# Kernel tuning notes

Measured on AMD Instinct MI355X. Metric: run time of the kernel, lower is better.

## Reference

```python
import jax, jax.numpy as jnp
import numpy as np

N_NODES = 16384
N_EDGES = 262144
D = 300
N_GRAPHS = 64


def setup_inputs() -> dict:
    key = jax.random.key(0)
    ks = jax.random.split(key, 16)
    s = 0.05  # small init scale for numerical stability
    inp = {
        "node_feats": jax.random.normal(ks[0], (N_NODES, D), jnp.float32),
        "W_lift": jax.random.normal(ks[1], (D, D), jnp.float32) * s,
        "b_lift": jnp.zeros((D,), jnp.float32),
        "Wf1": jax.random.normal(ks[2], (D, D), jnp.float32) * s,
        "bf1": jnp.zeros((D,), jnp.float32),
        "Wo1": jax.random.normal(ks[3], (D, D), jnp.float32) * s,
        "bo1": jnp.zeros((D,), jnp.float32),
        "Wf2": jax.random.normal(ks[4], (D, D), jnp.float32) * s,
        "bf2": jnp.zeros((D,), jnp.float32),
        "Wo2": jax.random.normal(ks[5], (D, D), jnp.float32) * s,
        "bo2": jnp.zeros((D,), jnp.float32),
        "Wf3": jax.random.normal(ks[6], (D, D), jnp.float32) * s,
        "bf3": jnp.zeros((D,), jnp.float32),
        "Wo3": jax.random.normal(ks[7], (D, D), jnp.float32) * s,
        "bo3": jnp.zeros((D,), jnp.float32),
        "W_ro": jax.random.normal(ks[8], (D, 2), jnp.float32) * s,
        "b_ro": jnp.zeros((2,), jnp.float32),
        "src": jax.random.randint(ks[9], (N_EDGES,), 0, N_NODES, jnp.int32),
        "dst": jax.random.randint(ks[10], (N_EDGES,), 0, N_NODES, jnp.int32),
        "graph_ids": jnp.sort(jax.random.randint(ks[11], (N_NODES,), 0, N_GRAPHS, jnp.int32)),
    }
    return inp


def _mp_layer(h, Wf, bf, Wo, bo, src, dst):
    # message: relu Dense on gathered src feats; reduce: segment-sum into dst nodes
    msg = jax.nn.relu(h[src] @ Wf + bf)                      # [E, D]
    agg = jax.ops.segment_sum(msg, dst, num_segments=N_NODES)  # [N, D]
    return jax.nn.relu(agg @ Wo + bo)                        # output Dense+ReLU


def reference(node_feats, W_lift, b_lift, Wf1, bf1, Wo1, bo1, Wf2, bf2, Wo2, bo2,
              Wf3, bf3, Wo3, bo3, W_ro, b_ro, src, dst, graph_ids):
    h = node_feats @ W_lift + b_lift  # lift, no activation
    h = _mp_layer(h, Wf1, bf1, Wo1, bo1, src, dst)
    h = _mp_layer(h, Wf2, bf2, Wo2, bo2, src, dst)
    h = _mp_layer(h, Wf3, bf3, Wo3, bo3, src, dst)
    probs = jax.nn.softmax(h @ W_ro + b_ro, axis=-1)         # readout Dense(softmax)
    logits = jax.ops.segment_sum(probs, graph_ids, num_segments=N_GRAPHS)  # dgl.sum_nodes
    return logits
```

## Files before the change

### kernel.cpp

```cpp
#include <hip/hip_runtime.h>
#include <hip/hip_bf16.h>

#define N_NODES 16384
#define N_EDGES 262144
#define GD 300
#define DP 320
#define N_GRAPHS 64
#define NTILE 5

typedef short bf16x8 __attribute__((ext_vector_type(8)));
typedef float f32x4 __attribute__((ext_vector_type(4)));

__device__ static inline unsigned short f2bf(float v) {
  __hip_bfloat16 b = __float2bfloat16(v);
  return __builtin_bit_cast(unsigned short, b);
}
__device__ static inline float bf2f(unsigned short u) {
  return __bfloat162float(__builtin_bit_cast(__hip_bfloat16, u));
}

#define GLOAD_LDS16(g, l)                                                    \
  __builtin_amdgcn_global_load_lds(                                          \
      (const __attribute__((address_space(1))) void*)(g),                    \
      (__attribute__((address_space(3))) void*)(l), 16, 0, 0)

constexpr int ATILE = 8192;
constexpr int AFULL = 5 * ATILE;
constexpr int BBUF = 40960;
constexpr int EPITCH = 328;
constexpr size_t WSZ = (size_t)DP * DP;
static_assert(64 * EPITCH * 2 <= AFULL + 2 * BBUF, "epilogue bounce fits");

template <bool RELU1, bool TILED, bool FUSE2, bool RO, bool CONVF>
__global__ __launch_bounds__(512, 2) void gemm_f(
    const unsigned short* __restrict__ A, const float* __restrict__ nf,
    const unsigned short* __restrict__ Wt1,
    const float* __restrict__ bias1, const unsigned short* __restrict__ Wt2,
    const float* __restrict__ bias2, unsigned short* __restrict__ C,
    const float* __restrict__ Wro, const float* __restrict__ bro,
    const int* __restrict__ gid, float* __restrict__ out) {
  __shared__ __align__(16) char smem[AFULL + 2 * BBUF];
  __shared__ float wroL[2 * DP];
  __shared__ float rowacc[2 * 64];
  __shared__ float binsL[2 * N_GRAPHS];

  const int bm = blockIdx.x * 64;
  const int t = threadIdx.x;
  const int w = t >> 6, l = t & 63;
  const int wr = w & 1;
  const int wc = w >> 1;
  const int cl = l & 15, q = l >> 4;
  const int lr = l >> 3;
  const int sg = (l & 7) ^ lr;

  if (RO) {
    for (int i = t; i < DP; i += 512) {
      wroL[2 * i] = (i < GD) ? Wro[2 * i] : 0.f;
      wroL[2 * i + 1] = (i < GD) ? Wro[2 * i + 1] : 0.f;
    }
    if (t < 128) rowacc[t] = 0.f;
    if (t < 2 * N_GRAPHS) binsL[t] = 0.f;
  }

  auto stageB = [&](const unsigned short* W, int tk, int buf) {
    char* lb = smem + AFULL + buf * BBUF;
#pragma unroll
    for (int i = 0; i < 5; ++i) {
      int c = w + 8 * i;
      GLOAD_LDS16(W + (size_t)(c * 8 + lr) * DP + tk * 64 + 8 * sg,
                  lb + c * 1024);
    }
  };

  f32x4 acc[2][5] = {};

  auto compute = [&](const char* lA, const char* lB) {
#pragma unroll
    for (int ks = 0; ks < 2; ++ks) {
      bf16x8 a[2], b[5];
#pragma unroll
      for (int m = 0; m < 2; ++m) {
        int r = wr * 32 + m * 16 + cl;
        int slot = (ks * 4 + q) ^ (r & 7);
        a[m] = *(const bf16x8*)(lA + r * 128 + slot * 16);
      }
#pragma unroll
      for (int n = 0; n < 5; ++n) {
        int r = wc * 80 + n * 16 + cl;
        int slot = (ks * 4 + q) ^ (r & 7);
        b[n] = *(const bf16x8*)(lB + r * 128 + slot * 16);
      }
#pragma unroll
      for (int m = 0; m < 2; ++m)
#pragma unroll
        for (int n = 0; n < 5; ++n)
          acc[m][n] = __builtin_amdgcn_mfma_f32_16x16x32_bf16(a[m], b[n],
                                                              acc[m][n], 0, 0, 0);
    }
  };

  stageB(Wt1, 0, 0);
  if (CONVF) {
    const int r = t >> 3;
    const int ls = t & 7;
    const float* rp = nf + (size_t)(bm + r) * GD;
#pragma unroll
    for (int p = 0; p < 5; ++p) {
      int c0 = p * 64 + ls * 8;
      bf16x8 o;
      if (c0 + 8 <= GD) {
        float4 a = *(const float4*)(rp + c0);
        float4 b = *(const float4*)(rp + c0 + 4);
        o[0] = f2bf(a.x); o[1] = f2bf(a.y); o[2] = f2bf(a.z); o[3] = f2bf(a.w);
        o[4] = f2bf(b.x); o[5] = f2bf(b.y); o[6] = f2bf(b.z); o[7] = f2bf(b.w);
      } else {
#pragma unroll
        for (int i = 0; i < 8; ++i) {
          int c = c0 + i;
          o[i] = f2bf(c < GD ? rp[c] : 0.f);
        }
      }
      *(bf16x8*)(smem + p * ATILE + r * 128 + ((ls ^ (r & 7)) << 4)) = o;
    }
    asm volatile("s_waitcnt lgkmcnt(0)" ::: "memory");
  } else {
#pragma unroll
    for (int p = 0; p < 5; ++p)
      GLOAD_LDS16(A + (size_t)(bm + w * 8 + lr) * DP + p * 64 + 8 * sg,
                  smem + p * ATILE + w * 1024);
  }

  for (int tk = 0; tk < 5; ++tk) {
    __builtin_amdgcn_s_barrier();
    if (tk + 1 < 5) {
      stageB(Wt1, tk + 1, (tk + 1) & 1);
      asm volatile("s_waitcnt vmcnt(5)" ::: "memory");
    } else {
      asm volatile("s_waitcnt vmcnt(0)" ::: "memory");
    }
    __builtin_amdgcn_s_barrier();
    compute(smem + tk * ATILE, smem + AFULL + (tk & 1) * BBUF);
  }

  if (FUSE2) {
    __syncthreads();
    stageB(Wt2, 0, 0);
#pragma unroll
    for (int n = 0; n < 5; ++n) {
      int col = wc * 80 + n * 16 + cl;
      float bv = bias1[col];
      int kt = col >> 6, kin = col & 63;
#pragma unroll
      for (int m = 0; m < 2; ++m) {
#pragma unroll
        for (int r = 0; r < 4; ++r) {
          int row = wr * 32 + m * 16 + q * 4 + r;
          float v = fmaxf(acc[m][n][r] + bv, 0.f);
          int byte = kt * ATILE + row * 128 + (((kin >> 3) ^ (row & 7)) << 4) +
                     ((kin & 7) << 1);
          *(unsigned short*)(smem + byte) = f2bf(v);
        }
      }
    }
    asm volatile("s_waitcnt lgkmcnt(0)" ::: "memory");
#pragma unroll
    for (int m = 0; m < 2; ++m)
#pragma unroll
      for (int n = 0; n < 5; ++n) acc[m][n] = f32x4{0.f, 0.f, 0.f, 0.f};

    for (int tk = 0; tk < 5; ++tk) {
      __builtin_amdgcn_s_barrier();
      if (tk + 1 < 5) {
        stageB(Wt2, tk + 1, (tk + 1) & 1);
        asm volatile("s_waitcnt vmcnt(5)" ::: "memory");
      } else {
        asm volatile("s_waitcnt vmcnt(0)" ::: "memory");
      }
      __builtin_amdgcn_s_barrier();
      compute(smem + tk * ATILE, smem + AFULL + (tk & 1) * BBUF);
    }
  }

  if (!RO) {
    const float* bp = FUSE2 ? bias2 : bias1;
    const bool relu = FUSE2 ? true : RELU1;
    __syncthreads();
    unsigned short* ep = (unsigned short*)smem;
#pragma unroll
    for (int n = 0; n < 5; ++n) {
      int col = wc * 80 + n * 16 + cl;
      float bv = bp[col];
#pragma unroll
      for (int m = 0; m < 2; ++m) {
#pragma unroll
        for (int r = 0; r < 4; ++r) {
          int row = wr * 32 + m * 16 + q * 4 + r;
          float v = acc[m][n][r] + bv;
          if (relu) v = fmaxf(v, 0.f);
          ep[row * EPITCH + col] = f2bf(v);
        }
      }
    }
    __syncthreads();
    {
      const int row = t >> 3, c0 = (t & 7) * 40;
#pragma unroll
      for (int gch = 0; gch < 5; ++gch) {
        int col = c0 + gch * 8;
        bf16x8 v = *(const bf16x8*)(ep + row * EPITCH + col);
        size_t idx;
        if (TILED)
          idx = ((size_t)(col >> 6) * N_NODES + (bm + row)) * 64 + (col & 63);
        else
          idx = (size_t)(bm + row) * DP + col;
        *(bf16x8*)(C + idx) = v;
      }
    }
  } else {
    float bv[5];
#pragma unroll
    for (int n = 0; n < 5; ++n) bv[n] = bias1[wc * 80 + n * 16 + cl];
#pragma unroll
    for (int m = 0; m < 2; ++m) {
#pragma unroll
      for (int r = 0; r < 4; ++r) {
        float s0 = 0.f, s1 = 0.f;
#pragma unroll
        for (int n = 0; n < 5; ++n) {
          int col = wc * 80 + n * 16 + cl;
          float v = fmaxf(acc[m][n][r] + bv[n], 0.f);
          s0 += v * wroL[2 * col];
          s1 += v * wroL[2 * col + 1];
        }
#pragma unroll
        for (int off = 1; off < 16; off <<= 1) {
          s0 += __shfl_xor(s0, off);
          s1 += __shfl_xor(s1, off);
        }
        if (cl == 0) {
          int row = wr * 32 + m * 16 + q * 4 + r;
          atomicAdd(&rowacc[2 * row], s0);
          atomicAdd(&rowacc[2 * row + 1], s1);
        }
      }
    }
    __syncthreads();
    if (t < 64) {
      float d0 = rowacc[2 * t] + bro[0];
      float d1 = rowacc[2 * t + 1] + bro[1];
      float mx = fmaxf(d0, d1);
      float e0 = expf(d0 - mx), e1 = expf(d1 - mx);
      float inv = 1.f / (e0 + e1);
      int g = gid[bm + t];
      atomicAdd(&binsL[2 * g], e0 * inv);
      atomicAdd(&binsL[2 * g + 1], e1 * inv);
    }
    __syncthreads();
    if (t < 2 * N_GRAPHS) {
      float v = binsL[t];
      if (v != 0.f) atomicAdd(&out[t], v);
    }
  }
}

__global__ void hist_kernel(const int* __restrict__ dst, int* __restrict__ cnt) {
  int e = blockIdx.x * blockDim.x + threadIdx.x;
  if (e < N_EDGES) atomicAdd(&cnt[dst[e]], 1);
}

__global__ __launch_bounds__(256) void scan_kernel(
    const int* __restrict__ cnt, int* __restrict__ row_ptr, int* __restrict__ row_fill,
    float* __restrict__ out, int out_n) {
  if (threadIdx.x < out_n) out[threadIdx.x] = 0.f;
  __shared__ int sums[256];
  const int t = threadIdx.x;
  const int base = t * 64;
  int loc[64];
#pragma unroll
  for (int i = 0; i < 16; ++i)
    *(int4*)&loc[i * 4] = *(const int4*)&cnt[base + i * 4];
  int s = 0;
#pragma unroll
  for (int i = 0; i < 64; ++i) s += loc[i];
  sums[t] = s;
  __syncthreads();
  for (int off = 1; off < 256; off <<= 1) {
    int x = (t >= off) ? sums[t - off] : 0;
    __syncthreads();
    sums[t] += x;
    __syncthreads();
  }
  int run = sums[t] - s;
  int rp[64];
#pragma unroll
  for (int i = 0; i < 64; ++i) {
    rp[i] = run;
    run += loc[i];
  }
#pragma unroll
  for (int i = 0; i < 16; ++i) {
    *(int4*)&row_ptr[base + i * 4] = *(const int4*)&rp[i * 4];
    *(int4*)&row_fill[base + i * 4] = *(const int4*)&rp[i * 4];
  }
  if (t == 255) row_ptr[N_NODES] = run;
}

__global__ void scatter_kernel(const int* __restrict__ src, const int* __restrict__ dst,
                               int* __restrict__ row_fill, int* __restrict__ csr_src) {
  int e = blockIdx.x * blockDim.x + threadIdx.x;
  if (e >= N_EDGES) return;
  int pos = atomicAdd(&row_fill[dst[e]], 1);
  csr_src[pos] = src[e];
}

__global__ __launch_bounds__(256) void spmm_tiled(
    const unsigned short* __restrict__ Mt, const int* __restrict__ row_ptr,
    const int* __restrict__ csr_src, unsigned short* __restrict__ agg) {
  const int tile = blockIdx.y;
  const int wv = threadIdx.x >> 6;
  const int l = threadIdx.x & 63;
  const int g = l >> 3;
  const int cs = l & 7;
  const int node = blockIdx.x * 32 + wv * 8 + g;
  const unsigned short* base = Mt + (size_t)tile * N_NODES * 64 + cs * 8;

  int j = row_ptr[node];
  const int j1 = row_ptr[node + 1];
  float acc[8] = {};
  for (; j + 8 <= j1; j += 8) {
    bf16x8 v[8];
#pragma unroll
    for (int u = 0; u < 8; ++u)
      v[u] = *(const bf16x8*)(base + (size_t)csr_src[j + u] * 64);
#pragma unroll
    for (int u = 0; u < 8; ++u)
#pragma unroll
      for (int i = 0; i < 8; ++i) acc[i] += bf2f(v[u][i]);
  }
  if (j + 4 <= j1) {
    bf16x8 v[4];
#pragma unroll
    for (int u = 0; u < 4; ++u)
      v[u] = *(const bf16x8*)(base + (size_t)csr_src[j + u] * 64);
#pragma unroll
    for (int u = 0; u < 4; ++u)
#pragma unroll
      for (int i = 0; i < 8; ++i) acc[i] += bf2f(v[u][i]);
    j += 4;
  }
  for (; j < j1; ++j) {
    bf16x8 v = *(const bf16x8*)(base + (size_t)csr_src[j] * 64);
#pragma unroll
    for (int i = 0; i < 8; ++i) acc[i] += bf2f(v[i]);
  }
  bf16x8 o;
#pragma unroll
  for (int i = 0; i < 8; ++i) o[i] = f2bf(acc[i]);
  *(bf16x8*)(agg + (size_t)node * DP + tile * 64 + cs * 8) = o;
}

struct WPtrs {
  const float* W[7];
  const float* b[5];
};

__global__ __launch_bounds__(256) void prep_kernel(
    WPtrs p, const float* __restrict__ bl, const float* __restrict__ bf1,
    unsigned short* __restrict__ Wt, float* __restrict__ biasP,
    int* __restrict__ cnt) {
  __shared__ unsigned short ld[64][33];
  const int t = threadIdx.x;
  const int wb = blockIdx.x;

  if (wb < 64) cnt[wb * 256 + t] = 0;

  if (wb >= 350) {
    __shared__ float red[4][64];
    const int b = wb - 350;
    const int nn = t & 63, jg = t >> 6;
    const int n = b * 64 + nn;
    const float* Wf1 = p.W[0];
    float s = 0.f;
    if (n < GD) {
      for (int j = jg; j < GD; j += 4) s += bl[j] * Wf1[(size_t)j * GD + n];
    }
    red[jg][nn] = s;
    __syncthreads();
    if (t < 64) {
      int nn2 = b * 64 + t;
      float v = red[0][t] + red[1][t] + red[2][t] + red[3][t];
      biasP[nn2] = (nn2 < GD) ? v + bf1[nn2] : 0.f;
      biasP[DP + nn2] = 0.f;
    }
    return;
  }

  const int wi = wb / 50;
  const int blk = wb - wi * 50;
  const int kt = blk / 5;
  const int nt = blk - kt * 5;
  const int k0 = kt * 32, n0 = nt * 64;
  const float* W = p.W[wi];

  if (wi == 6) {
#pragma unroll
    for (int ps = 0; ps < 8; ++ps) {
      int idx = t + 256 * ps;
      int rr = idx >> 6, cc = idx & 63;
      float v = (k0 + rr < GD && n0 + cc < GD) ? W[(size_t)(k0 + rr) * GD + n0 + cc] : 0.f;
      Wt[2 * WSZ + (size_t)(k0 + rr) * DP + n0 + cc] = f2bf(v);
    }
    return;
  }
  const int slot = (wi == 0) ? 1 : wi + 2;
#pragma unroll
  for (int ps = 0; ps < 8; ++ps) {
    int idx = t + 256 * ps;
    int rr = idx >> 6, cc = idx & 63;
    float v = (k0 + rr < GD && n0 + cc < GD) ? W[(size_t)(k0 + rr) * GD + n0 + cc] : 0.f;
    ld[cc][rr] = f2bf(v);
  }
  __syncthreads();
#pragma unroll
  for (int ps = 0; ps < 8; ++ps) {
    int idx = t + 256 * ps;
    int nn = idx >> 5, kk = idx & 31;
    Wt[(size_t)slot * WSZ + (size_t)(n0 + nn) * DP + k0 + kk] = ld[nn][kk];
  }
  if (blk == 0 && wi >= 1) {
    for (int i = t; i < DP; i += 256)
      biasP[(size_t)(wi + 2) * DP + i] = (i < GD) ? p.b[wi - 1][i] : 0.f;
  }
}

extern "C" void kernel_launch(void* const* d_in, const int* in_sizes, int n_in,
                              void* d_out, int out_size, void* d_ws, size_t ws_size,
                              hipStream_t stream) {
  const float* node_feats = (const float*)d_in[0];
  const float* W_lift = (const float*)d_in[1];
  const float* b_lift = (const float*)d_in[2];
  const float* Wf1 = (const float*)d_in[3];
  const float* bf1 = (const float*)d_in[4];
  const float* W_ro = (const float*)d_in[15];
  const float* b_ro = (const float*)d_in[16];
  const int* src = (const int*)d_in[17];
  const int* dst = (const int*)d_in[18];
  const int* gid = (const int*)d_in[19];
  float* out = (float*)d_out;

  WPtrs wp;
  wp.W[0] = Wf1;
  wp.W[1] = (const float*)d_in[5];   wp.b[0] = (const float*)d_in[6];
  wp.W[2] = (const float*)d_in[7];   wp.b[1] = (const float*)d_in[8];
  wp.W[3] = (const float*)d_in[9];   wp.b[2] = (const float*)d_in[10];
  wp.W[4] = (const float*)d_in[11];  wp.b[3] = (const float*)d_in[12];
  wp.W[5] = (const float*)d_in[13];  wp.b[4] = (const float*)d_in[14];
  wp.W[6] = W_lift;

  char* p = (char*)d_ws;
  unsigned short* X = (unsigned short*)p;  p += (size_t)N_NODES * DP * 2;
  unsigned short* Y = (unsigned short*)p;  p += (size_t)N_NODES * DP * 2;
  unsigned short* Wt = (unsigned short*)p; p += (size_t)8 * WSZ * 2;
  float* biasP = (float*)p;                p += 8 * DP * 4;
  int* cnt = (int*)p;                      p += N_NODES * 4;
  int* row_ptr = (int*)p;                  p += (N_NODES + 16) * 4;
  int* row_fill = (int*)p;                 p += N_NODES * 4;
  int* csr_src = (int*)p;                  p += N_EDGES * 4;

  prep_kernel<<<355, 256, 0, stream>>>(wp, b_lift, bf1, Wt, biasP, cnt);
  hist_kernel<<<N_EDGES / 256, 256, 0, stream>>>(dst, cnt);
  scan_kernel<<<1, 256, 0, stream>>>(cnt, row_ptr, row_fill, out, out_size);
  scatter_kernel<<<N_EDGES / 256, 256, 0, stream>>>(src, dst, row_fill, csr_src);

  gemm_f<false, false, false, false, false><<<5, 512, 0, stream>>>(
      Wt + 1 * WSZ, nullptr, Wt + 2 * WSZ, biasP + 1 * DP, nullptr, nullptr,
      Wt + 0 * WSZ, nullptr, nullptr, nullptr, nullptr);

  dim3 sgrid(N_NODES / 32, NTILE);

  gemm_f<true, true, false, false, true><<<256, 512, 0, stream>>>(
      nullptr, node_feats, Wt + 0 * WSZ, biasP + 0 * DP, nullptr, nullptr, Y,
      nullptr, nullptr, nullptr, nullptr);
  spmm_tiled<<<sgrid, 256, 0, stream>>>(Y, row_ptr, csr_src, X);
  gemm_f<true, true, true, false, false><<<256, 512, 0, stream>>>(
      X, nullptr, Wt + 3 * WSZ, biasP + 3 * DP, Wt + 4 * WSZ, biasP + 4 * DP, Y,
      nullptr, nullptr, nullptr, nullptr);
  spmm_tiled<<<sgrid, 256, 0, stream>>>(Y, row_ptr, csr_src, X);
  gemm_f<true, true, true, false, false><<<256, 512, 0, stream>>>(
      X, nullptr, Wt + 5 * WSZ, biasP + 5 * DP, Wt + 6 * WSZ, biasP + 6 * DP, Y,
      nullptr, nullptr, nullptr, nullptr);
  spmm_tiled<<<sgrid, 256, 0, stream>>>(Y, row_ptr, csr_src, X);
  gemm_f<true, false, false, true, false><<<256, 512, 0, stream>>>(
      X, nullptr, Wt + 7 * WSZ, biasP + 7 * DP, nullptr, nullptr, nullptr,
      W_ro, b_ro, gid, out);
}
```

Measured before the change: 192.4 us.

## Fuse CSR segment-sum gather into GEMM A-tile staging, drop spmm kernels

Removes the three standalone spmm_tiled kernels and makes the following GEMM gather and sum neighbor rows directly into its LDS A tiles, one k-tile at a time, overlapped with B staging. This avoids writing the aggregated matrix to global memory and reading it back, and saves three kernel launches. In exchange, the GEMM grid of 256 blocks now carries the irregular gather latency inside its main loop, which may serialize with the MFMA work and cut the parallelism the dedicated spmm grid had.

```diff
diff --git a/kernel.cpp b/kernel.cpp
--- a/kernel.cpp
+++ b/kernel.cpp
@@ -31,9 +31,10 @@
 constexpr size_t WSZ = (size_t)DP * DP;
 static_assert(64 * EPITCH * 2 <= AFULL + 2 * BBUF, "epilogue bounce fits");
 
-template <bool RELU1, bool TILED, bool FUSE2, bool RO, bool CONVF>
+template <bool RELU1, bool TILED, bool FUSE2, bool RO, bool CONVF, bool AGG>
 __global__ __launch_bounds__(512, 2) void gemm_f(
     const unsigned short* __restrict__ A, const float* __restrict__ nf,
+    const int* __restrict__ row_ptr, const int* __restrict__ csr,
     const unsigned short* __restrict__ Wt1,
     const float* __restrict__ bias1, const unsigned short* __restrict__ Wt2,
     const float* __restrict__ bias2, unsigned short* __restrict__ C,
@@ -62,6 +63,13 @@
     if (t < 2 * N_GRAPHS) binsL[t] = 0.f;
   }
 
+  int j0 = 0, j1 = 0;
+  if (AGG) {
+    int node = bm + (t >> 3);
+    j0 = row_ptr[node];
+    j1 = row_ptr[node + 1];
+  }
+
   auto stageB = [&](const unsigned short* W, int tk, int buf) {
     char* lb = smem + AFULL + buf * BBUF;
 #pragma unroll
@@ -70,6 +78,43 @@
       GLOAD_LDS16(W + (size_t)(c * 8 + lr) * DP + tk * 64 + 8 * sg,
                   lb + c * 1024);
     }
+  };
+
+  auto gatherA = [&](int tk) {
+    const unsigned short* base = A + (size_t)tk * N_NODES * 64 + (t & 7) * 8;
+    float a8[8] = {};
+    int j = j0;
+    for (; j + 8 <= j1; j += 8) {
+      bf16x8 v[8];
+#pragma unroll
+      for (int u = 0; u < 8; ++u)
+        v[u] = *(const bf16x8*)(base + (size_t)csr[j + u] * 64);
+#pragma unroll
+      for (int u = 0; u < 8; ++u)
+#pragma unroll
+        for (int i = 0; i < 8; ++i) a8[i] += bf2f(v[u][i]);
+    }
+    if (j + 4 <= j1) {
+      bf16x8 v[4];
+#pragma unroll
+      for (int u = 0; u < 4; ++u)
+        v[u] = *(const bf16x8*)(base + (size_t)csr[j + u] * 64);
+#pragma unroll
+      for (int u = 0; u < 4; ++u)
+#pragma unroll
+        for (int i = 0; i < 8; ++i) a8[i] += bf2f(v[u][i]);
+      j += 4;
+    }
+    for (; j < j1; ++j) {
+      bf16x8 v = *(const bf16x8*)(base + (size_t)csr[j] * 64);
+#pragma unroll
+      for (int i = 0; i < 8; ++i) a8[i] += bf2f(v[i]);
+    }
+    bf16x8 o;
+#pragma unroll
+    for (int i = 0; i < 8; ++i) o[i] = f2bf(a8[i]);
+    const int g = t >> 3, e = t & 7;
+    *(bf16x8*)(smem + tk * ATILE + g * 128 + ((e ^ (g & 7)) << 4)) = o;
   };
 
   f32x4 acc[2][5] = {};
@@ -123,6 +168,9 @@
       *(bf16x8*)(smem + p * ATILE + r * 128 + ((ls ^ (r & 7)) << 4)) = o;
     }
     asm volatile("s_waitcnt lgkmcnt(0)" ::: "memory");
+  } else if (AGG) {
+    gatherA(0);
+    asm volatile("s_waitcnt lgkmcnt(0)" ::: "memory");
   } else {
 #pragma unroll
     for (int p = 0; p < 5; ++p)
@@ -134,6 +182,10 @@
     __builtin_amdgcn_s_barrier();
     if (tk + 1 < 5) {
       stageB(Wt1, tk + 1, (tk + 1) & 1);
+      if (AGG) {
+        gatherA(tk + 1);
+        asm volatile("s_waitcnt lgkmcnt(0)" ::: "memory");
+      }
       asm volatile("s_waitcnt vmcnt(5)" ::: "memory");
     } else {
       asm volatile("s_waitcnt vmcnt(0)" ::: "memory");
@@ -311,52 +363,6 @@
   if (e >= N_EDGES) return;
   int pos = atomicAdd(&row_fill[dst[e]], 1);
   csr_src[pos] = src[e];
-}
-
-__global__ __launch_bounds__(256) void spmm_tiled(
-    const unsigned short* __restrict__ Mt, const int* __restrict__ row_ptr,
-    const int* __restrict__ csr_src, unsigned short* __restrict__ agg) {
-  const int tile = blockIdx.y;
-  const int wv = threadIdx.x >> 6;
-  const int l = threadIdx.x & 63;
-  const int g = l >> 3;
-  const int cs = l & 7;
-  const int node = blockIdx.x * 32 + wv * 8 + g;
-  const unsigned short* base = Mt + (size_t)tile * N_NODES * 64 + cs * 8;
-
-  int j = row_ptr[node];
-  const int j1 = row_ptr[node + 1];
-  float acc[8] = {};
-  for (; j + 8 <= j1; j += 8) {
-    bf16x8 v[8];
-#pragma unroll
-    for (int u = 0; u < 8; ++u)
-      v[u] = *(const bf16x8*)(base + (size_t)csr_src[j + u] * 64);
-#pragma unroll
-    for (int u = 0; u < 8; ++u)
-#pragma unroll
-      for (int i = 0; i < 8; ++i) acc[i] += bf2f(v[u][i]);
-  }
-  if (j + 4 <= j1) {
-    bf16x8 v[4];
-#pragma unroll
-    for (int u = 0; u < 4; ++u)
-      v[u] = *(const bf16x8*)(base + (size_t)csr_src[j + u] * 64);
-#pragma unroll
-    for (int u = 0; u < 4; ++u)
-#pragma unroll
-      for (int i = 0; i < 8; ++i) acc[i] += bf2f(v[u][i]);
-    j += 4;
-  }
-  for (; j < j1; ++j) {
-    bf16x8 v = *(const bf16x8*)(base + (size_t)csr_src[j] * 64);
-#pragma unroll
-    for (int i = 0; i < 8; ++i) acc[i] += bf2f(v[i]);
-  }
-  bf16x8 o;
-#pragma unroll
-  for (int i = 0; i < 8; ++i) o[i] = f2bf(acc[i]);
-  *(bf16x8*)(agg + (size_t)node * DP + tile * 64 + cs * 8) = o;
 }
 
 struct WPtrs {
@@ -472,25 +478,20 @@
   scan_kernel<<<1, 256, 0, stream>>>(cnt, row_ptr, row_fill, out, out_size);
   scatter_kernel<<<N_EDGES / 256, 256, 0, stream>>>(src, dst, row_fill, csr_src);
 
-  gemm_f<false, false, false, false, false><<<5, 512, 0, stream>>>(
-      Wt + 1 * WSZ, nullptr, Wt + 2 * WSZ, biasP + 1 * DP, nullptr, nullptr,
-      Wt + 0 * WSZ, nullptr, nullptr, nullptr, nullptr);
-
-  dim3 sgrid(N_NODES / 32, NTILE);
-
-  gemm_f<true, true, false, false, true><<<256, 512, 0, stream>>>(
-      nullptr, node_feats, Wt + 0 * WSZ, biasP + 0 * DP, nullptr, nullptr, Y,
-      nullptr, nullptr, nullptr, nullptr);
-  spmm_tiled<<<sgrid, 256, 0, stream>>>(Y, row_ptr, csr_src, X);
-  gemm_f<true, true, true, false, false><<<256, 512, 0, stream>>>(
-      X, nullptr, Wt + 3 * WSZ, biasP + 3 * DP, Wt + 4 * WSZ, biasP + 4 * DP, Y,
-      nullptr, nullptr, nullptr, nullptr);
-  spmm_tiled<<<sgrid, 256, 0, stream>>>(Y, row_ptr, csr_src, X);
-  gemm_f<true, true, true, false, false><<<256, 512, 0, stream>>>(
-      X, nullptr, Wt + 5 * WSZ, biasP + 5 * DP, Wt + 6 * WSZ, biasP + 6 * DP, Y,
-      nullptr, nullptr, nullptr, nullptr);
-  spmm_tiled<<<sgrid, 256, 0, stream>>>(Y, row_ptr, csr_src, X);
-  gemm_f<true, false, false, true, false><<<256, 512, 0, stream>>>(
-      X, nullptr, Wt + 7 * WSZ, biasP + 7 * DP, nullptr, nullptr, nullptr,
-      W_ro, b_ro, gid, out);
-}
+  gemm_f<false, false, false, false, false, false><<<5, 512, 0, stream>>>(
+      Wt + 1 * WSZ, nullptr, nullptr, nullptr, Wt + 2 * WSZ, biasP + 1 * DP,
+      nullptr, nullptr, Wt + 0 * WSZ, nullptr, nullptr, nullptr, nullptr);
+
+  gemm_f<true, true, false, false, true, false><<<256, 512, 0, stream>>>(
+      nullptr, node_feats, nullptr, nullptr, Wt + 0 * WSZ, biasP + 0 * DP,
+      nullptr, nullptr, Y, nullptr, nullptr, nullptr, nullptr);
+  gemm_f<true, true, true, false, false, true><<<256, 512, 0, stream>>>(
+      Y, nullptr, row_ptr, csr_src, Wt + 3 * WSZ, biasP + 3 * DP,
+      Wt + 4 * WSZ, biasP + 4 * DP, X, nullptr, nullptr, nullptr, nullptr);
+  gemm_f<true, true, true, false, false, true><<<256, 512, 0, stream>>>(
+      X, nullptr, row_ptr, csr_src, Wt + 5 * WSZ, biasP + 5 * DP,
+      Wt + 6 * WSZ, biasP + 6 * DP, Y, nullptr, nullptr, nullptr, nullptr);
+  gemm_f<true, false, false, true, false, true><<<256, 512, 0, stream>>>(
+      Y, nullptr, row_ptr, csr_src, Wt + 7 * WSZ, biasP + 7 * DP,
+      nullptr, nullptr, nullptr, W_ro, b_ro, gid, out);
+}
```

After: 203.6 us. +5.8%, slower.

## Single-buffer weight tiles via register prefetch to raise GEMM occupancy

Applied to the files above, without the earlier changes.

Replaces the double-buffered direct-to-LDS weight staging with a register prefetch of the next K-tile, written into a single LDS buffer after compute. The readout scratch arrays move into reused shared memory. This cuts LDS per block so the launch bound can rise to four blocks per CU for better latency hiding. In exchange it adds register pressure from the prefetch buffers, an extra barrier and LDS store per tile, and register spill risk at the higher occupancy target.

```diff
diff --git a/kernel.cpp b/kernel.cpp
--- a/kernel.cpp
+++ b/kernel.cpp
@@ -29,20 +29,17 @@
 constexpr int BBUF = 40960;
 constexpr int EPITCH = 328;
 constexpr size_t WSZ = (size_t)DP * DP;
-static_assert(64 * EPITCH * 2 <= AFULL + 2 * BBUF, "epilogue bounce fits");
+static_assert(64 * EPITCH * 2 <= AFULL + BBUF, "epilogue bounce fits");
 
 template <bool RELU1, bool TILED, bool FUSE2, bool RO, bool CONVF>
-__global__ __launch_bounds__(512, 2) void gemm_f(
+__global__ __launch_bounds__(512, 4) void gemm_f(
     const unsigned short* __restrict__ A, const float* __restrict__ nf,
     const unsigned short* __restrict__ Wt1,
     const float* __restrict__ bias1, const unsigned short* __restrict__ Wt2,
     const float* __restrict__ bias2, unsigned short* __restrict__ C,
     const float* __restrict__ Wro, const float* __restrict__ bro,
     const int* __restrict__ gid, float* __restrict__ out) {
-  __shared__ __align__(16) char smem[AFULL + 2 * BBUF];
-  __shared__ float wroL[2 * DP];
-  __shared__ float rowacc[2 * 64];
-  __shared__ float binsL[2 * N_GRAPHS];
+  __shared__ __align__(16) char smem[AFULL + BBUF];
 
   const int bm = blockIdx.x * 64;
   const int t = threadIdx.x;
@@ -53,28 +50,27 @@
   const int lr = l >> 3;
   const int sg = (l & 7) ^ lr;
 
-  if (RO) {
-    for (int i = t; i < DP; i += 512) {
-      wroL[2 * i] = (i < GD) ? Wro[2 * i] : 0.f;
-      wroL[2 * i + 1] = (i < GD) ? Wro[2 * i + 1] : 0.f;
-    }
-    if (t < 128) rowacc[t] = 0.f;
-    if (t < 2 * N_GRAPHS) binsL[t] = 0.f;
-  }
-
-  auto stageB = [&](const unsigned short* W, int tk, int buf) {
-    char* lb = smem + AFULL + buf * BBUF;
+  bf16x8 breg[5];
+  auto loadBreg = [&](const unsigned short* W, int tk) {
 #pragma unroll
     for (int i = 0; i < 5; ++i) {
       int c = w + 8 * i;
-      GLOAD_LDS16(W + (size_t)(c * 8 + lr) * DP + tk * 64 + 8 * sg,
-                  lb + c * 1024);
+      breg[i] = *(const bf16x8*)(W + (size_t)(c * 8 + lr) * DP + tk * 64 + 8 * sg);
     }
   };
+  auto writeBlds = [&]() {
+    char* lb = smem + AFULL;
+#pragma unroll
+    for (int i = 0; i < 5; ++i) {
+      int c = w + 8 * i;
+      *(bf16x8*)(lb + c * 1024 + (l & 7) * 16 + lr * 128) = breg[i];
+    }
+  };
 
   f32x4 acc[2][5] = {};
 
-  auto compute = [&](const char* lA, const char* lB) {
+  auto compute = [&](const char* lA) {
+    const char* lB = smem + AFULL;
 #pragma unroll
     for (int ks = 0; ks < 2; ++ks) {
       bf16x8 a[2], b[5];
@@ -99,7 +95,7 @@
     }
   };
 
-  stageB(Wt1, 0, 0);
+  loadBreg(Wt1, 0);
   if (CONVF) {
     const int r = t >> 3;
     const int ls = t & 7;
@@ -122,29 +118,26 @@
       }
       *(bf16x8*)(smem + p * ATILE + r * 128 + ((ls ^ (r & 7)) << 4)) = o;
     }
-    asm volatile("s_waitcnt lgkmcnt(0)" ::: "memory");
   } else {
 #pragma unroll
     for (int p = 0; p < 5; ++p)
       GLOAD_LDS16(A + (size_t)(bm + w * 8 + lr) * DP + p * 64 + 8 * sg,
                   smem + p * ATILE + w * 1024);
   }
+  asm volatile("s_waitcnt vmcnt(0)" ::: "memory");
+  writeBlds();
 
   for (int tk = 0; tk < 5; ++tk) {
+    asm volatile("s_waitcnt lgkmcnt(0)" ::: "memory");
     __builtin_amdgcn_s_barrier();
-    if (tk + 1 < 5) {
-      stageB(Wt1, tk + 1, (tk + 1) & 1);
-      asm volatile("s_waitcnt vmcnt(5)" ::: "memory");
-    } else {
-      asm volatile("s_waitcnt vmcnt(0)" ::: "memory");
-    }
+    if (tk + 1 < 5) loadBreg(Wt1, tk + 1);
+    compute(smem + tk * ATILE);
     __builtin_amdgcn_s_barrier();
-    compute(smem + tk * ATILE, smem + AFULL + (tk & 1) * BBUF);
+    if (tk + 1 < 5) writeBlds();
   }
 
   if (FUSE2) {
-    __syncthreads();
-    stageB(Wt2, 0, 0);
+    loadBreg(Wt2, 0);
 #pragma unroll
     for (int n = 0; n < 5; ++n) {
       int col = wc * 80 + n * 16 + cl;
@@ -162,22 +155,19 @@
         }
       }
     }
-    asm volatile("s_waitcnt lgkmcnt(0)" ::: "memory");
+    writeBlds();
 #pragma unroll
     for (int m = 0; m < 2; ++m)
 #pragma unroll
       for (int n = 0; n < 5; ++n) acc[m][n] = f32x4{0.f, 0.f, 0.f, 0.f};
 
     for (int tk = 0; tk < 5; ++tk) {
+      asm volatile("s_waitcnt lgkmcnt(0)" ::: "memory");
       __builtin_amdgcn_s_barrier();
-      if (tk + 1 < 5) {
-        stageB(Wt2, tk + 1, (tk + 1) & 1);
-        asm volatile("s_waitcnt vmcnt(5)" ::: "memory");
-      } else {
-        asm volatile("s_waitcnt vmcnt(0)" ::: "memory");
-      }
+      if (tk + 1 < 5) loadBreg(Wt2, tk + 1);
+      compute(smem + tk * ATILE);
       __builtin_amdgcn_s_barrier();
-      compute(smem + tk * ATILE, smem + AFULL + (tk & 1) * BBUF);
+      if (tk + 1 < 5) writeBlds();
     }
   }
 
@@ -217,6 +207,18 @@
       }
     }
   } else {
+    __syncthreads();
+    float* wroL = (float*)smem;
+    float* rowacc = wroL + 2 * DP;
+    float* binsL = rowacc + 128;
+    for (int i = t; i < DP; i += 512) {
+      wroL[2 * i] = (i < GD) ? Wro[2 * i] : 0.f;
+      wroL[2 * i + 1] = (i < GD) ? Wro[2 * i + 1] : 0.f;
+    }
+    if (t < 128) rowacc[t] = 0.f;
+    if (t >= 128 && t < 256) binsL[t - 128] = 0.f;
+    __syncthreads();
+
     float bv[5];
 #pragma unroll
     for (int n = 0; n < 5; ++n) bv[n] = bias1[wc * 80 + n * 16 + cl];
```

New measurement: 203.3 us. +5.7%, slower.
